# Kernel tuning notes

Hardware: AMD Instinct MI355X
Metric: run time of the kernel (lower is better)

Reference implementation:

```python
import jax, jax.numpy as jnp
import numpy as np

B, T, H, K = 4, 1024, 1024, 16
HD = H // K  # head dim
EPS = 1e-5


def _layernorm(x, g, b):
    mu = jnp.mean(x, axis=-1, keepdims=True)
    var = jnp.mean(jnp.square(x - mu), axis=-1, keepdims=True)
    return (x - mu) * jax.lax.rsqrt(var + EPS) * g + b


def setup_inputs() -> dict:
    key = jax.random.key(0)
    ks = jax.random.split(key, 16)
    s = 0.02
    return {
        "x": jax.random.normal(ks[0], (B, T, H), jnp.float32),
        "ln1_g": jnp.ones((H,), jnp.float32),
        "ln1_b": jnp.zeros((H,), jnp.float32),
        "ln2_g": jnp.ones((H,), jnp.float32),
        "ln2_b": jnp.zeros((H,), jnp.float32),
        "Wq": jax.random.normal(ks[1], (H, H), jnp.float32) * s,
        "bq": jnp.zeros((H,), jnp.float32),
        "Wk": jax.random.normal(ks[2], (H, H), jnp.float32) * s,
        "bk": jnp.zeros((H,), jnp.float32),
        "Wv": jax.random.normal(ks[3], (H, H), jnp.float32) * s,
        "bv": jnp.zeros((H,), jnp.float32),
        "W1": jax.random.normal(ks[4], (H, 4 * H), jnp.float32) * s,
        "b1": jnp.zeros((4 * H,), jnp.float32),
        "W2": jax.random.normal(ks[5], (4 * H, H), jnp.float32) * s,
        "b2": jnp.zeros((H,), jnp.float32),
    }


def reference(x, ln1_g, ln1_b, ln2_g, ln2_b, Wq, bq, Wk, bk, Wv, bv, W1, b1, W2, b2):
    # --- attention sub-block ---
    h = _layernorm(x, ln1_g, ln1_b)                      # (B,T,H)
    q = (h @ Wq + bq).reshape(B, T, K, HD).transpose(0, 2, 1, 3)  # (B,K,T,hd)
    k = (h @ Wk + bk).reshape(B, T, K, HD).transpose(0, 2, 1, 3)
    v = (h @ Wv + bv).reshape(B, T, K, HD).transpose(0, 2, 1, 3)
    qkt = jnp.einsum('bkqd,bkpd->bkqp', q, k)            # (B,K,T,T)
    attn = qkt * (1.0 / np.sqrt(HD))
    # module quirk: masked positions are FILLED with 1e-9 (not -inf) before softmax
    causal_mask = jnp.triu(jnp.ones((T, T), bool), k=1)  # True above diagonal = masked
    attn = jnp.where(causal_mask, jnp.float32(1e-9), attn)
    attn = jax.nn.softmax(attn, axis=-1)
    y = jnp.einsum('bkqp,bkpd->bkqd', attn, v)           # (B,K,T,hd)
    y = y.transpose(0, 2, 1, 3).reshape(B, T, H)
    x = x + y
    # --- MLP sub-block (dropout is identity at eval) ---
    h2 = _layernorm(x, ln2_g, ln2_b)
    m = jax.nn.gelu(h2 @ W1 + b1, approximate=False) @ W2 + b2
    return x + m
```

## Files before the change

kernel.cpp:

```cpp
#include <hip/hip_runtime.h>
#include <hip/hip_bf16.h>
#include <math.h>


typedef __attribute__((ext_vector_type(8))) short bf16x8;
typedef __attribute__((ext_vector_type(4))) float f32x4;

#define DEVINL __device__ __forceinline__

#define LOG2E_SCALE 0.18033688f
#define MASK2 1.4426950408889634e-9f

DEVINL void stage16(const __hip_bfloat16* g, short* l) {
  __builtin_amdgcn_global_load_lds(
      (const __attribute__((address_space(1))) unsigned int*)g,
      (__attribute__((address_space(3))) unsigned int*)l, 16, 0, 0);
}

DEVINL float bf2f(short u) {
  unsigned x = ((unsigned)(unsigned short)u) << 16;
  float f; __builtin_memcpy(&f, &x, 4); return f;
}

DEVINL short f2bf_s(float f) {
  __hip_bfloat16 h = __float2bfloat16(f);
  short s; __builtin_memcpy(&s, &h, 2); return s;
}

DEVINL float block_sum(float v, float* sb) {
  #pragma unroll
  for (int o = 32; o; o >>= 1) v += __shfl_down(v, o);
  const int lane = threadIdx.x & 63, w = threadIdx.x >> 6;
  if (lane == 0) sb[w] = v;
  __syncthreads();
  float r = sb[0] + sb[1] + sb[2] + sb[3];
  __syncthreads();
  return r;
}

template<int BM, int BN, int WM, int WN>
DEVINL void gemm_core64(const __hip_bfloat16* __restrict__ A, int lda,
                        const __hip_bfloat16* __restrict__ Bt, int ldb,
                        int Kd, int row0, int col0,
                        f32x4 (&acc)[WM/16][WN/16],
                        short* lds_a, short* lds_b) {
  constexpr int MI = WM / 16, NI = WN / 16, WNC = BN / WN;
  constexpr int CA = BM * 8, CB = BN * 8;
  const int tid = threadIdx.x;
  const int lane = tid & 63, wave = tid >> 6;
  const int wm = (wave / WNC) * WM, wn = (wave % WNC) * WN;
  const int lr = lane & 15, lq = lane >> 4;
  for (int k0 = 0; k0 < Kd; k0 += 64) {
    #pragma unroll
    for (int c = tid; c < CA; c += 256) {
      const int r = c >> 3, kc = ((c & 7) ^ (r & 7)) << 3;
      stage16(A + (size_t)(row0 + r) * lda + k0 + kc, lds_a + c * 8);
    }
    #pragma unroll
    for (int c = tid; c < CB; c += 256) {
      const int r = c >> 3, kc = ((c & 7) ^ (r & 7)) << 3;
      stage16(Bt + (size_t)(col0 + r) * ldb + k0 + kc, lds_b + c * 8);
    }
    __syncthreads();
    #pragma unroll
    for (int s = 0; s < 2; s++) {
      bf16x8 af[MI], bfr[NI];
      #pragma unroll
      for (int mi = 0; mi < MI; mi++) {
        const int m = wm + mi * 16 + lr;
        af[mi] = *(const bf16x8*)(lds_a + m * 64 + (((s * 4 + lq) ^ (m & 7)) << 3));
      }
      #pragma unroll
      for (int ni = 0; ni < NI; ni++) {
        const int n = wn + ni * 16 + lr;
        bfr[ni] = *(const bf16x8*)(lds_b + n * 64 + (((s * 4 + lq) ^ (n & 7)) << 3));
      }
      #pragma unroll
      for (int mi = 0; mi < MI; mi++)
        #pragma unroll
        for (int ni = 0; ni < NI; ni++)
          acc[mi][ni] = __builtin_amdgcn_mfma_f32_16x16x32_bf16(
              af[mi], bfr[ni], acc[mi][ni], 0, 0, 0);
    }
    __syncthreads();
  }
}

__global__ __launch_bounds__(256) void k_tcvt(const float* __restrict__ src,
                                              __hip_bfloat16* __restrict__ dst,
                                              int R, int C, int dstOff, int dstPitch) {
  __shared__ float tile[32][33];
  const int c0 = blockIdx.x * 32, r0 = blockIdx.y * 32;
  const int tx = threadIdx.x, ty = threadIdx.y;
  #pragma unroll
  for (int i = 0; i < 32; i += 8)
    tile[ty + i][tx] = src[(size_t)(r0 + ty + i) * C + c0 + tx];
  __syncthreads();
  #pragma unroll
  for (int i = 0; i < 32; i += 8)
    dst[(size_t)(c0 + ty + i + dstOff) * dstPitch + r0 + tx] =
        __float2bfloat16(tile[tx][ty + i]);
}

__global__ __launch_bounds__(256) void k_tcvt3(const float* __restrict__ Wq,
                                               const float* __restrict__ Wk,
                                               const float* __restrict__ Wv,
                                               __hip_bfloat16* __restrict__ dst) {
  __shared__ float tile[32][33];
  const float* src = blockIdx.z == 0 ? Wq : (blockIdx.z == 1 ? Wk : Wv);
  const int dstOff = blockIdx.z << 10;
  const int c0 = blockIdx.x * 32, r0 = blockIdx.y * 32;
  const int tx = threadIdx.x, ty = threadIdx.y;
  #pragma unroll
  for (int i = 0; i < 32; i += 8)
    tile[ty + i][tx] = src[(size_t)(r0 + ty + i) * 1024 + c0 + tx];
  __syncthreads();
  #pragma unroll
  for (int i = 0; i < 32; i += 8)
    dst[(size_t)(c0 + ty + i + dstOff) * 1024 + r0 + tx] =
        __float2bfloat16(tile[tx][ty + i]);
}

__global__ __launch_bounds__(256) void k_pack_bias(const float* __restrict__ bq,
                                                   const float* __restrict__ bk,
                                                   const float* __restrict__ bv,
                                                   float* __restrict__ o) {
  const int i = blockIdx.x * 256 + threadIdx.x;
  if (i < 3072)
    o[i] = i < 1024 ? bq[i] : (i < 2048 ? bk[i - 1024] : bv[i - 2048]);
}

__global__ __launch_bounds__(256) void k_ln(const float* __restrict__ x,
                                            const float* __restrict__ y,
                                            const float* __restrict__ g,
                                            const float* __restrict__ bb,
                                            __hip_bfloat16* __restrict__ o,
                                            const float* __restrict__ badd,
                                            float* __restrict__ oinit) {
  __shared__ float sb[4];
  const int t = threadIdx.x;
  const size_t base = (size_t)blockIdx.x * 1024 + t * 4;
  const int c = t * 4;
  float4 xv = *(const float4*)(x + base);
  if (y) {
    float4 yv = *(const float4*)(y + base);
    xv.x += yv.x; xv.y += yv.y; xv.z += yv.z; xv.w += yv.w;
    float4 ov;
    ov.x = xv.x + badd[c + 0]; ov.y = xv.y + badd[c + 1];
    ov.z = xv.z + badd[c + 2]; ov.w = xv.w + badd[c + 3];
    *(float4*)(oinit + base) = ov;
  }
  const float mu = block_sum(xv.x + xv.y + xv.z + xv.w, sb) * (1.f / 1024.f);
  const float dx = xv.x - mu, dy = xv.y - mu, dz = xv.z - mu, dw = xv.w - mu;
  const float var = block_sum(dx * dx + dy * dy + dz * dz + dw * dw, sb) * (1.f / 1024.f);
  const float rs = rsqrtf(var + 1e-5f);
  o[base + 0] = __float2bfloat16(dx * rs * g[c + 0] + bb[c + 0]);
  o[base + 1] = __float2bfloat16(dy * rs * g[c + 1] + bb[c + 1]);
  o[base + 2] = __float2bfloat16(dz * rs * g[c + 2] + bb[c + 2]);
  o[base + 3] = __float2bfloat16(dw * rs * g[c + 3] + bb[c + 3]);
}

__global__ __launch_bounds__(256) void k_gemm_qkv(
    const __hip_bfloat16* __restrict__ h1, const __hip_bfloat16* __restrict__ Wt,
    const float* __restrict__ bqkv, __hip_bfloat16* __restrict__ Q,
    __hip_bfloat16* __restrict__ K, __hip_bfloat16* __restrict__ Vt) {
  __shared__ alignas(16) short smem[16896];
  short* la = smem;
  short* lb = smem + 8192;
  short* lc = smem;
  const int row0 = blockIdx.x * 128, col0 = blockIdx.y * 128;
  f32x4 acc[4][4] = {};
  gemm_core64<128, 128, 64, 64>(h1, 1024, Wt, 1024, 1024, row0, col0, acc, la, lb);
  const int tid = threadIdx.x, lane = tid & 63, wave = tid >> 6;
  const int wm = (wave >> 1) * 64, wn = (wave & 1) * 64, lr = lane & 15, lq = lane >> 4;
  const int which = col0 >> 10;
  const int h0 = (col0 & 1023) >> 6;
  const int b = row0 >> 10, t0 = row0 & 1023;
  if (which < 2) {
    const float qs = (which == 0) ? LOG2E_SCALE : 1.f;
    #pragma unroll
    for (int mi = 0; mi < 4; mi++)
      #pragma unroll
      for (int ni = 0; ni < 4; ni++)
        #pragma unroll
        for (int r = 0; r < 4; r++) {
          const int row = wm + mi * 16 + lq * 4 + r;
          const int col = wn + ni * 16 + lr;
          lc[row * 132 + col] = f2bf_s((acc[mi][ni][r] + bqkv[col0 + col]) * qs);
        }
    __syncthreads();
    __hip_bfloat16* O = which == 0 ? Q : K;
    #pragma unroll
    for (int c = 0; c < 8; c++) {
      const int f = tid + 256 * c;
      const int r = f >> 4, cc = f & 15;
      const int col = cc * 8;
      const int head = h0 + (col >> 6), d = col & 63;
      float4 vv = *(const float4*)(lc + r * 132 + col);
      *(float4*)(O + (((size_t)(b * 16 + head)) << 16) + (t0 + r) * 64 + d) = vv;
    }
  } else {
    #pragma unroll
    for (int mi = 0; mi < 4; mi++)
      #pragma unroll
      for (int ni = 0; ni < 4; ni++)
        #pragma unroll
        for (int r = 0; r < 4; r++) {
          const int row = wm + mi * 16 + lq * 4 + r;
          const int col = wn + ni * 16 + lr;
          lc[col * 132 + row] = f2bf_s(acc[mi][ni][r] + bqkv[col0 + col]);
        }
    __syncthreads();
    #pragma unroll
    for (int c = 0; c < 8; c++) {
      const int f = tid + 256 * c;
      const int dl = f >> 4, tc = f & 15;
      const int head = h0 + (dl >> 6), d = dl & 63;
      float4 vv = *(const float4*)(lc + dl * 132 + tc * 8);
      *(float4*)(Vt + (((size_t)(b * 16 + head)) << 16) + (size_t)d * 1024 +
                 t0 + tc * 8) = vv;
    }
  }
}

__global__ __launch_bounds__(256) void k_tailv(const __hip_bfloat16* __restrict__ Vt,
                                               float* __restrict__ TV) {
  __shared__ float ts[8][64];
  const int hb = blockIdx.x, tid = threadIdx.x;
  const __hip_bfloat16* Vh = Vt + ((size_t)hb << 16);
  for (int w = tid; w < 512; w += 256) {
    const int kt = w >> 6, d = w & 63;
    const short* p = (const short*)(Vh + (size_t)d * 1024 + kt * 128);
    float s = 0.f;
    for (int j = 0; j < 128; j += 8) {
      bf16x8 v = *(const bf16x8*)(p + j);
      #pragma unroll
      for (int e = 0; e < 8; e++) s += bf2f(v[e]);
    }
    ts[kt][d] = s;
  }
  __syncthreads();
  for (int w = tid; w < 512; w += 256) {
    const int qt = w >> 6, d = w & 63;
    float s = 0.f;
    for (int kt = qt + 1; kt < 8; kt++) s += ts[kt][d];
    TV[((size_t)hb * 8 + qt) * 64 + d] = s;
  }
}

__global__ __launch_bounds__(256, 3) void k_attn(
    const __hip_bfloat16* __restrict__ Q, const __hip_bfloat16* __restrict__ K,
    const __hip_bfloat16* __restrict__ Vt, const float* __restrict__ TV,
    float* __restrict__ y) {
  __shared__ short lp[64 * 130];
  __shared__ short lK[128 * 64];
  __shared__ short lV[128 * 64];
  const int hb = blockIdx.y;
  const int j = (blockIdx.y & 32) ? (15 - (int)blockIdx.x) : (int)blockIdx.x;
  const int q0 = j * 64;
  const int nkt = (j >> 1) + 1;
  const int tid = threadIdx.x, lane = tid & 63, wave = tid >> 6;
  const int lr = lane & 15, lq = lane >> 4;
  const int wm = wave * 16;
  const __hip_bfloat16* Qh = Q + ((size_t)hb << 16);
  const __hip_bfloat16* Kh = K + ((size_t)hb << 16);
  const __hip_bfloat16* Vh = Vt + ((size_t)hb << 16);

  bf16x8 qf[2];
  #pragma unroll
  for (int s = 0; s < 2; s++)
    qf[s] = *(const bf16x8*)((const short*)Qh +
                             (size_t)(q0 + wm + lr) * 64 + s * 32 + lq * 8);

  f32x4 oacc[4] = {};
  float mrow[4], lrow[4];
  #pragma unroll
  for (int r = 0; r < 4; r++) { mrow[r] = -1e30f; lrow[r] = 0.f; }

  for (int c = tid; c < 1024; c += 256)
    stage16(Kh + (size_t)(c >> 3) * 64 + (((c & 7) ^ ((c >> 3) & 7)) << 3),
            lK + c * 8);
  __syncthreads();

  for (int kt = 0; kt < nkt; kt++) {
    const int k0 = kt * 128;
    f32x4 sacc[8] = {};
    __builtin_amdgcn_s_setprio(1);
    #pragma unroll
    for (int s = 0; s < 2; s++) {
      bf16x8 bf[8];
      #pragma unroll
      for (int ni = 0; ni < 8; ni++) {
        const int n = ni * 16 + lr;
        bf[ni] = *(const bf16x8*)(lK + n * 64 + (((s * 4 + lq) ^ (n & 7)) << 3));
      }
      #pragma unroll
      for (int ni = 0; ni < 8; ni++)
        sacc[ni] = __builtin_amdgcn_mfma_f32_16x16x32_bf16(
            qf[s], bf[ni], sacc[ni], 0, 0, 0);
    }
    __builtin_amdgcn_s_setprio(0);
    __syncthreads();
    for (int c = tid; c < 1024; c += 256)
      stage16(Vh + (size_t)(c >> 4) * 1024 + k0 + (((c & 15) ^ ((c >> 4) & 15)) << 3),
              lV + c * 8);
    if (kt + 1 < nkt) {
      const int k1 = k0 + 128;
      for (int c = tid; c < 1024; c += 256)
        stage16(Kh + (size_t)(k1 + (c >> 3)) * 64 + (((c & 7) ^ ((c >> 3) & 7)) << 3),
                lK + c * 8);
    }
    const bool last = (kt == nkt - 1);
    #pragma unroll
    for (int r = 0; r < 4; r++) {
      const int grow = q0 + wm + lq * 4 + r;
      float tmax = -1e30f;
      #pragma unroll
      for (int ni = 0; ni < 8; ni++) {
        float v = sacc[ni][r];
        if (last && (k0 + ni * 16 + lr) > grow) v = MASK2;
        sacc[ni][r] = v;
        tmax = fmaxf(tmax, v);
      }
      #pragma unroll
      for (int msk = 8; msk; msk >>= 1) tmax = fmaxf(tmax, __shfl_xor(tmax, msk));
      const float mn = fmaxf(mrow[r], tmax);
      const float al = __builtin_amdgcn_exp2f(mrow[r] - mn);
      float rs = 0.f;
      #pragma unroll
      for (int ni = 0; ni < 8; ni++) {
        const float pv = __builtin_amdgcn_exp2f(sacc[ni][r] - mn);
        sacc[ni][r] = pv;
        rs += pv;
      }
      #pragma unroll
      for (int msk = 8; msk; msk >>= 1) rs += __shfl_xor(rs, msk);
      mrow[r] = mn;
      lrow[r] = lrow[r] * al + rs;
      #pragma unroll
      for (int ni = 0; ni < 4; ni++) oacc[ni][r] *= al;
    }
    #pragma unroll
    for (int r = 0; r < 4; r++) {
      const int row = wm + lq * 4 + r;
      #pragma unroll
      for (int ni = 0; ni < 8; ni++)
        lp[row * 130 + ni * 16 + lr] = f2bf_s(sacc[ni][r]);
    }
    __syncthreads();
    __builtin_amdgcn_s_setprio(1);
    #pragma unroll
    for (int ks = 0; ks < 4; ks++) {
      bf16x8 pa, vb[4];
      pa = *(const bf16x8*)(lp + (wm + lr) * 130 + ks * 32 + lq * 8);
      #pragma unroll
      for (int ni = 0; ni < 4; ni++) {
        const int d = ni * 16 + lr;
        vb[ni] = *(const bf16x8*)(lV + d * 128 + (((ks * 4 + lq) ^ (d & 15)) << 3));
      }
      #pragma unroll
      for (int ni = 0; ni < 4; ni++)
        oacc[ni] = __builtin_amdgcn_mfma_f32_16x16x32_bf16(
            pa, vb[ni], oacc[ni], 0, 0, 0);
    }
    __builtin_amdgcn_s_setprio(0);
  }

  const int b = hb >> 4, h = hb & 15;
  const float cv = (float)(1024 - nkt * 128);
  const float* tv = TV + ((size_t)hb * 8 + (j >> 1)) * 64;
  #pragma unroll
  for (int r = 0; r < 4; r++) {
    const int t = q0 + wm + lq * 4 + r;
    const float tail = __builtin_amdgcn_exp2f(MASK2 - mrow[r]);
    const float inv = 1.f / (lrow[r] + cv * tail);
    #pragma unroll
    for (int ni = 0; ni < 4; ni++) {
      const int d = ni * 16 + lr;
      y[((size_t)(b * 1024 + t) << 10) + h * 64 + d] =
          (oacc[ni][r] + tail * tv[d]) * inv;
    }
  }
}

template<int MH, int NH>
DEVINL void ph_read(const short* pa, const short* pb, int wr, int wc,
                    int lr, int lq, bf16x8 (&af)[4][2], bf16x8 (&bf)[2][2]) {
  if (NH == 0) {
    #pragma unroll
    for (int mi2 = 0; mi2 < 4; mi2++)
      #pragma unroll
      for (int ks = 0; ks < 2; ks++) {
        const int r = wr * 128 + MH * 64 + mi2 * 16 + lr;
        af[mi2][ks] = *(const bf16x8*)(pa + r * 64 + (((ks * 4 + lq) ^ (r & 7)) << 3));
      }
  }
  #pragma unroll
  for (int ni2 = 0; ni2 < 2; ni2++)
    #pragma unroll
    for (int ks = 0; ks < 2; ks++) {
      const int n = wc * 64 + NH * 32 + ni2 * 16 + lr;
      bf[ni2][ks] = *(const bf16x8*)(pb + n * 64 + (((ks * 4 + lq) ^ (n & 7)) << 3));
    }
}

DEVINL void ph_sync() {
  __builtin_amdgcn_s_barrier();
  asm volatile("s_waitcnt lgkmcnt(0)" ::: "memory");
  __builtin_amdgcn_sched_barrier(0);
}

template<int MH, int NH>
DEVINL void ph_mfma(f32x4 (&acc)[8][4], bf16x8 (&af)[4][2], bf16x8 (&bf)[2][2]) {
  __builtin_amdgcn_s_setprio(1);
  #pragma unroll
  for (int mi2 = 0; mi2 < 4; mi2++)
    #pragma unroll
    for (int ni2 = 0; ni2 < 2; ni2++)
      #pragma unroll
      for (int ks = 0; ks < 2; ks++)
        acc[MH * 4 + mi2][NH * 2 + ni2] = __builtin_amdgcn_mfma_f32_16x16x32_bf16(
            af[mi2][ks], bf[ni2][ks], acc[MH * 4 + mi2][NH * 2 + ni2], 0, 0, 0);
  __builtin_amdgcn_s_setprio(0);
  __builtin_amdgcn_s_barrier();
}

__global__ __launch_bounds__(512, 2) void k_gemm_mlp1(const __hip_bfloat16* __restrict__ h2,
                                                      const __hip_bfloat16* __restrict__ W1t,
                                                      const float* __restrict__ b1,
                                                      __hip_bfloat16* __restrict__ G) {
  __shared__ alignas(16) short smem[65536];
  short* Ae = smem;
  short* Ao = smem + 16384;
  short* Be = smem + 32768;
  short* Bo = smem + 49152;
  const int row0 = blockIdx.x * 256, col0 = blockIdx.y * 256;
  const int tid = threadIdx.x, lane = tid & 63, wid = tid >> 6;
  const int lr = lane & 15, lq = lane >> 4;
  const int wr = wid >> 2, wc = wid & 3;
  const __hip_bfloat16* A = h2 + (size_t)row0 * 1024;
  const __hip_bfloat16* Bt = W1t + (size_t)col0 * 1024;

  auto STG = [&](const __hip_bfloat16* src, int k0, int h, short* dst, int SH) {
    #pragma unroll
    for (int ii = 0; ii < 2; ii++) {
      const int f = tid + ii * 512;
      const int rp = f >> 3, P = f & 7;
      const int r = ((rp >> SH) << (SH + 1)) | (h << SH) | (rp & ((1 << SH) - 1));
      const int g = P ^ (r & 7);
      stage16(src + (size_t)r * 1024 + k0 + g * 8, dst + r * 64 + P * 8);
    }
  };

  f32x4 acc[8][4] = {};
  bf16x8 af[4][2], bf[2][2];

  STG(A, 0, 0, Ae, 6);  STG(Bt, 0, 0, Be, 5);
  STG(A, 0, 1, Ae, 6);  STG(Bt, 0, 1, Be, 5);
  STG(A, 64, 0, Ao, 6); STG(Bt, 64, 0, Bo, 5);
  asm volatile("s_waitcnt vmcnt(4)" ::: "memory");
  __syncthreads();

  for (int i = 0; i < 8; ++i) {
    const int kE1 = (i + 1) * 128;
    const int kO0 = i * 128 + 64;
    const int kO1 = kE1 + 64;
    const bool more = (i + 1 < 8);
    ph_read<0, 0>(Ae, Be, wr, wc, lr, lq, af, bf);
    STG(A, kO0, 1, Ao, 6);
    ph_sync();
    ph_mfma<0, 0>(acc, af, bf);
    ph_read<0, 1>(Ae, Be, wr, wc, lr, lq, af, bf);
    STG(Bt, kO0, 1, Bo, 5);
    ph_sync();
    ph_mfma<0, 1>(acc, af, bf);
    ph_read<1, 0>(Ae, Be, wr, wc, lr, lq, af, bf);
    if (more) STG(A, kE1, 0, Ae, 6);
    ph_sync();
    ph_mfma<1, 0>(acc, af, bf);
    ph_read<1, 1>(Ae, Be, wr, wc, lr, lq, af, bf);
    if (more) {
      STG(Bt, kE1, 0, Be, 5);
      asm volatile("s_waitcnt vmcnt(4)" ::: "memory");
    } else {
      asm volatile("s_waitcnt vmcnt(0)" ::: "memory");
    }
    ph_sync();
    ph_mfma<1, 1>(acc, af, bf);
    ph_read<0, 0>(Ao, Bo, wr, wc, lr, lq, af, bf);
    if (more) STG(A, kE1, 1, Ae, 6);
    ph_sync();
    ph_mfma<0, 0>(acc, af, bf);
    ph_read<0, 1>(Ao, Bo, wr, wc, lr, lq, af, bf);
    if (more) STG(Bt, kE1, 1, Be, 5);
    ph_sync();
    ph_mfma<0, 1>(acc, af, bf);
    ph_read<1, 0>(Ao, Bo, wr, wc, lr, lq, af, bf);
    if (more) STG(A, kO1, 0, Ao, 6);
    ph_sync();
    ph_mfma<1, 0>(acc, af, bf);
    ph_read<1, 1>(Ao, Bo, wr, wc, lr, lq, af, bf);
    if (more) {
      STG(Bt, kO1, 0, Bo, 5);
      asm volatile("s_waitcnt vmcnt(4)" ::: "memory");
    }
    ph_sync();
    ph_mfma<1, 1>(acc, af, bf);
  }

  short* lc = smem;
  #pragma unroll
  for (int pr = 0; pr < 4; pr++) {
    if ((wid >> 2) == (pr >> 1)) {
      const int mib = (pr & 1) * 4;
      #pragma unroll
      for (int mi2 = 0; mi2 < 4; mi2++)
        #pragma unroll
        for (int ni = 0; ni < 4; ni++)
          #pragma unroll
          for (int rr = 0; rr < 4; rr++) {
            const int rloc = mi2 * 16 + lq * 4 + rr;
            const int col = (wid & 3) * 64 + ni * 16 + lr;
            float v = acc[mib + mi2][ni][rr] + b1[col0 + col];
            const float u2 = fminf(v * (2.3022079f + 0.1029434f * v * v), 80.f);
            const float e = __builtin_amdgcn_exp2f(u2);
            v = v * e * __builtin_amdgcn_rcpf(e + 1.f);
            lc[rloc * 264 + col] = f2bf_s(v);
          }
    }
    __syncthreads();
    #pragma unroll
    for (int c = 0; c < 4; c++) {
      const int f = tid + 512 * c;
      const int r = f >> 5, cc = f & 31;
      float4 vv = *(const float4*)(lc + r * 264 + cc * 8);
      *(float4*)(G + ((size_t)(row0 + pr * 64 + r) << 12) + col0 + cc * 8) = vv;
    }
    __syncthreads();
  }
}

__global__ __launch_bounds__(256) void k_gemm_mlp2(const __hip_bfloat16* __restrict__ G,
                                                   const __hip_bfloat16* __restrict__ W2t,
                                                   float* __restrict__ out) {
  __shared__ alignas(16) short smem[12288];
  short* la = smem;
  short* lb = smem + 8192;
  const int row0 = blockIdx.x * 128, col0 = blockIdx.y * 64;
  const int kOff = blockIdx.z * 2048;
  f32x4 acc[4][2] = {};
  gemm_core64<128, 64, 64, 32>(G + kOff, 4096, W2t + kOff, 4096, 2048,
                               row0, col0, acc, la, lb);
  const int lane = threadIdx.x & 63, wave = threadIdx.x >> 6;
  const int wm = (wave >> 1) * 64, wn = (wave & 1) * 32, lr = lane & 15, lq = lane >> 4;
  #pragma unroll
  for (int mi = 0; mi < 4; mi++)
    #pragma unroll
    for (int ni = 0; ni < 2; ni++)
      #pragma unroll
      for (int r = 0; r < 4; r++) {
        const int grow = row0 + wm + mi * 16 + lq * 4 + r;
        const int gcol = col0 + wn + ni * 16 + lr;
        atomicAdd(out + (((size_t)grow << 10) + gcol), acc[mi][ni][r]);
      }
}

extern "C" void kernel_launch(void* const* d_in, const int* in_sizes, int n_in,
                              void* d_out, int out_size, void* d_ws, size_t ws_size,
                              hipStream_t stream) {
  const float* x     = (const float*)d_in[0];
  const float* ln1_g = (const float*)d_in[1];
  const float* ln1_b = (const float*)d_in[2];
  const float* ln2_g = (const float*)d_in[3];
  const float* ln2_b = (const float*)d_in[4];
  const float* Wq    = (const float*)d_in[5];
  const float* bq    = (const float*)d_in[6];
  const float* Wk    = (const float*)d_in[7];
  const float* bk    = (const float*)d_in[8];
  const float* Wv    = (const float*)d_in[9];
  const float* bv    = (const float*)d_in[10];
  const float* W1    = (const float*)d_in[11];
  const float* b1    = (const float*)d_in[12];
  const float* W2    = (const float*)d_in[13];
  const float* b2    = (const float*)d_in[14];
  float* out = (float*)d_out;

  char* p = (char*)d_ws;
  auto alloc = [&](size_t bytes) { char* r = p; p += (bytes + 255) & ~(size_t)255; return r; };
  __hip_bfloat16* wqkv = (__hip_bfloat16*)alloc(3072 * 1024 * 2);
  __hip_bfloat16* w1t  = (__hip_bfloat16*)alloc(4096 * 1024 * 2);
  __hip_bfloat16* w2t  = (__hip_bfloat16*)alloc(1024 * 4096 * 2);
  float*          bqkv = (float*)alloc(3072 * 4);
  __hip_bfloat16* h1   = (__hip_bfloat16*)alloc(4096 * 1024 * 2);
  __hip_bfloat16* Qb   = (__hip_bfloat16*)alloc((size_t)64 * 65536 * 2);
  __hip_bfloat16* Kb   = (__hip_bfloat16*)alloc((size_t)64 * 65536 * 2);
  __hip_bfloat16* Vt   = (__hip_bfloat16*)alloc((size_t)64 * 65536 * 2);
  float*          TV   = (float*)alloc((size_t)64 * 8 * 64 * 4);
  float*          yb   = (float*)alloc((size_t)4096 * 1024 * 4);
  __hip_bfloat16* h2   = (__hip_bfloat16*)alloc(4096 * 1024 * 2);
  __hip_bfloat16* G    = (__hip_bfloat16*)alloc((size_t)4096 * 4096 * 2);
  (void)ws_size; (void)in_sizes; (void)n_in; (void)out_size;

  const dim3 b256(256), bt(32, 8);
  k_tcvt3<<<dim3(32, 32, 3), bt, 0, stream>>>(Wq, Wk, Wv, wqkv);
  k_tcvt<<<dim3(128, 32), bt, 0, stream>>>(W1, w1t, 1024, 4096, 0, 1024);
  k_tcvt<<<dim3(32, 128), bt, 0, stream>>>(W2, w2t, 4096, 1024, 0, 4096);
  k_pack_bias<<<12, b256, 0, stream>>>(bq, bk, bv, bqkv);

  k_ln<<<4096, b256, 0, stream>>>(x, nullptr, ln1_g, ln1_b, h1, nullptr, nullptr);
  k_gemm_qkv<<<dim3(32, 24), b256, 0, stream>>>(h1, wqkv, bqkv, Qb, Kb, Vt);
  k_tailv<<<64, b256, 0, stream>>>(Vt, TV);
  k_attn<<<dim3(16, 64), b256, 0, stream>>>(Qb, Kb, Vt, TV, yb);

  k_ln<<<4096, b256, 0, stream>>>(x, yb, ln2_g, ln2_b, h2, b2, out);
  k_gemm_mlp1<<<dim3(16, 16), dim3(512), 0, stream>>>(h2, w1t, b1, G);
  k_gemm_mlp2<<<dim3(32, 16, 2), b256, 0, stream>>>(G, w2t, out);
}
```

Measured before the change: 329.6 us.

## Rewrite MLP2 GEMM with larger tiles and ping-pong LDS pipeline

Replaces the generic 128x64 gemm_core64 path for the second MLP GEMM with a dedicated 256x128-tile, 512-thread kernel. It double-buffers even/odd K-slices in LDS with XOR-swizzled direct global-to-LDS loads, and interleaves half-tile MFMA phases with explicit vmcnt waits and priority hints. The aim is more operand reuse per load, fewer atomics per output, and overlap of memory with compute. The trade-off is far fewer blocks (256 instead of 1024), which can leave CUs underused, plus 96KB of LDS per block.

```diff
diff --git a/kernel.cpp b/kernel.cpp
--- a/kernel.cpp
+++ b/kernel.cpp
@@ -540,28 +540,124 @@
   }
 }
 
-__global__ __launch_bounds__(256) void k_gemm_mlp2(const __hip_bfloat16* __restrict__ G,
-                                                   const __hip_bfloat16* __restrict__ W2t,
-                                                   float* __restrict__ out) {
-  __shared__ alignas(16) short smem[12288];
-  short* la = smem;
-  short* lb = smem + 8192;
-  const int row0 = blockIdx.x * 128, col0 = blockIdx.y * 64;
+template<int MH>
+DEVINL void mm2(f32x4 (&acc)[4][4], bf16x8 (&af)[2][2], bf16x8 (&bf)[4][2]) {
+  __builtin_amdgcn_s_setprio(1);
+  #pragma unroll
+  for (int mi2 = 0; mi2 < 2; mi2++)
+    #pragma unroll
+    for (int ni = 0; ni < 4; ni++)
+      #pragma unroll
+      for (int ks = 0; ks < 2; ks++)
+        acc[MH * 2 + mi2][ni] = __builtin_amdgcn_mfma_f32_16x16x32_bf16(
+            af[mi2][ks], bf[ni][ks], acc[MH * 2 + mi2][ni], 0, 0, 0);
+  __builtin_amdgcn_s_setprio(0);
+  __builtin_amdgcn_s_barrier();
+}
+
+__global__ __launch_bounds__(512, 2) void k_gemm_mlp2(const __hip_bfloat16* __restrict__ G,
+                                                      const __hip_bfloat16* __restrict__ W2t,
+                                                      float* __restrict__ out) {
+  __shared__ alignas(16) short smem[49152];
+  short* Ae = smem;
+  short* Ao = smem + 16384;
+  short* Be = smem + 32768;
+  short* Bo = smem + 40960;
+  const int row0 = blockIdx.x * 256, col0 = blockIdx.y * 128;
   const int kOff = blockIdx.z * 2048;
-  f32x4 acc[4][2] = {};
-  gemm_core64<128, 64, 64, 32>(G + kOff, 4096, W2t + kOff, 4096, 2048,
-                               row0, col0, acc, la, lb);
-  const int lane = threadIdx.x & 63, wave = threadIdx.x >> 6;
-  const int wm = (wave >> 1) * 64, wn = (wave & 1) * 32, lr = lane & 15, lq = lane >> 4;
+  const int tid = threadIdx.x, lane = tid & 63, wid = tid >> 6;
+  const int lr = lane & 15, lq = lane >> 4;
+  const int wr = wid >> 1, wc = wid & 1;
+  const __hip_bfloat16* A = G + (size_t)row0 * 4096 + kOff;
+  const __hip_bfloat16* Bt = W2t + (size_t)col0 * 4096 + kOff;
+
+  auto STGA = [&](int k0, int h, short* dst) {
+    #pragma unroll
+    for (int ii = 0; ii < 2; ii++) {
+      const int f = tid + ii * 512;
+      const int rp = f >> 3, P = f & 7;
+      const int r = ((rp >> 5) << 6) | (h << 5) | (rp & 31);
+      const int g = P ^ (r & 7);
+      stage16(A + (size_t)r * 4096 + k0 + g * 8, dst + r * 64 + P * 8);
+    }
+  };
+  auto STGB = [&](int k0, short* dst) {
+    #pragma unroll
+    for (int ii = 0; ii < 2; ii++) {
+      const int f = tid + ii * 512;
+      const int r = f >> 3, P = f & 7;
+      const int g = P ^ (r & 7);
+      stage16(Bt + (size_t)r * 4096 + k0 + g * 8, dst + r * 64 + P * 8);
+    }
+  };
+
+  f32x4 acc[4][4] = {};
+  bf16x8 af[2][2], bf[4][2];
+
+  auto RDA = [&](const short* pa, int MH) {
+    #pragma unroll
+    for (int mi2 = 0; mi2 < 2; mi2++)
+      #pragma unroll
+      for (int ks = 0; ks < 2; ks++) {
+        const int r = wr * 64 + MH * 32 + mi2 * 16 + lr;
+        af[mi2][ks] = *(const bf16x8*)(pa + r * 64 + (((ks * 4 + lq) ^ (r & 7)) << 3));
+      }
+  };
+  auto RDB = [&](const short* pb) {
+    #pragma unroll
+    for (int ni = 0; ni < 4; ni++)
+      #pragma unroll
+      for (int ks = 0; ks < 2; ks++) {
+        const int n = wc * 64 + ni * 16 + lr;
+        bf[ni][ks] = *(const bf16x8*)(pb + n * 64 + (((ks * 4 + lq) ^ (n & 7)) << 3));
+      }
+  };
+
+  STGB(0, Be); STGA(0, 0, Ae);
+  STGA(0, 1, Ae);
+  STGB(64, Bo); STGA(64, 0, Ao);
+  asm volatile("s_waitcnt vmcnt(4)" ::: "memory");
+  __syncthreads();
+
+  for (int i = 0; i < 16; ++i) {
+    const int kE1 = (i + 1) * 128, kO0 = i * 128 + 64, kO1 = kE1 + 64;
+    const bool more = (i + 1 < 16);
+    RDA(Ae, 0); RDB(Be);
+    STGA(kO0, 1, Ao);
+    asm volatile("s_waitcnt vmcnt(2)" ::: "memory");
+    ph_sync();
+    mm2<0>(acc, af, bf);
+    RDA(Ae, 1);
+    if (more) { STGB(kE1, Be); STGA(kE1, 0, Ae); }
+    ph_sync();
+    mm2<1>(acc, af, bf);
+    RDA(Ao, 0); RDB(Bo);
+    if (more) {
+      STGA(kE1, 1, Ae);
+      asm volatile("s_waitcnt vmcnt(6)" ::: "memory");
+    } else {
+      asm volatile("s_waitcnt vmcnt(0)" ::: "memory");
+    }
+    ph_sync();
+    mm2<0>(acc, af, bf);
+    RDA(Ao, 1);
+    if (more) {
+      STGB(kO1, Bo); STGA(kO1, 0, Ao);
+      asm volatile("s_waitcnt vmcnt(4)" ::: "memory");
+    }
+    ph_sync();
+    mm2<1>(acc, af, bf);
+  }
+
   #pragma unroll
   for (int mi = 0; mi < 4; mi++)
     #pragma unroll
-    for (int ni = 0; ni < 2; ni++)
-      #pragma unroll
-      for (int r = 0; r < 4; r++) {
-        const int grow = row0 + wm + mi * 16 + lq * 4 + r;
-        const int gcol = col0 + wn + ni * 16 + lr;
-        atomicAdd(out + (((size_t)grow << 10) + gcol), acc[mi][ni][r]);
+    for (int ni = 0; ni < 4; ni++)
+      #pragma unroll
+      for (int rr = 0; rr < 4; rr++) {
+        const int grow = row0 + wr * 64 + mi * 16 + lq * 4 + rr;
+        const int gcol = col0 + wc * 64 + ni * 16 + lr;
+        atomicAdd(out + (((size_t)grow << 10) + gcol), acc[mi][ni][rr]);
       }
 }
 
@@ -614,5 +710,5 @@
 
   k_ln<<<4096, b256, 0, stream>>>(x, yb, ln2_g, ln2_b, h2, b2, out);
   k_gemm_mlp1<<<dim3(16, 16), dim3(512), 0, stream>>>(h2, w1t, b1, G);
-  k_gemm_mlp2<<<dim3(32, 16, 2), b256, 0, stream>>>(G, w2t, out);
-}
+  k_gemm_mlp2<<<dim3(16, 8, 2), dim3(512), 0, stream>>>(G, w2t, out);
+}
```

Measured after the change: 328.4 us. Within noise of the previous version (-0.4%).
